# Kernel optimization log

Measured on AMD Instinct MI355X. Metric: run time of the kernel, lower is better.

## Reference

```python
import jax, jax.numpy as jnp
import numpy as np

HIDDEN = 896
N_HEADS = 14
N_KV = 2
HEAD_DIM = HIDDEN // N_HEADS  # 64
N_REP = N_HEADS // N_KV       # 7
ROPE_THETA = 1000000.0


def setup_inputs() -> dict:
    key = jax.random.key(0)
    ks = jax.random.split(key, 8)
    B, S = 2, 2048
    s = 0.02
    return {
        "hidden_states": jax.random.normal(ks[0], (B, S, HIDDEN), dtype=jnp.float32),
        "position_ids": jnp.broadcast_to(jnp.arange(S, dtype=jnp.int64), (B, S)),
        "Wq": jax.random.normal(ks[1], (HIDDEN, HIDDEN), dtype=jnp.float32) * s,
        "bq": jnp.zeros((HIDDEN,), dtype=jnp.float32),
        "Wk": jax.random.normal(ks[2], (N_KV * HEAD_DIM, HIDDEN), dtype=jnp.float32) * s,
        "bk": jnp.zeros((N_KV * HEAD_DIM,), dtype=jnp.float32),
        "Wv": jax.random.normal(ks[3], (N_KV * HEAD_DIM, HIDDEN), dtype=jnp.float32) * s,
        "bv": jnp.zeros((N_KV * HEAD_DIM,), dtype=jnp.float32),
        "Wo": jax.random.normal(ks[4], (HIDDEN, HIDDEN), dtype=jnp.float32) * s,
    }


def _rotate_half(x):
    x1, x2 = x[..., : HEAD_DIM // 2], x[..., HEAD_DIM // 2 :]
    return jnp.concatenate((-x2, x1), axis=-1)


def reference(hidden_states, position_ids, Wq, bq, Wk, bk, Wv, bv, Wo):
    B, S, _ = hidden_states.shape
    q = (hidden_states @ Wq.T + bq).reshape(B, S, N_HEADS, HEAD_DIM)
    k = (hidden_states @ Wk.T + bk).reshape(B, S, N_KV, HEAD_DIM)
    v = (hidden_states @ Wv.T + bv).reshape(B, S, N_KV, HEAD_DIM)

    # RoPE: cos/sin [B, S, 1, HEAD_DIM]
    inv_freq = 1.0 / (ROPE_THETA ** (jnp.arange(0, HEAD_DIM, 2, dtype=jnp.float32) / HEAD_DIM))
    freqs = position_ids.astype(jnp.float32)[..., None] * inv_freq  # [B,S,D/2]
    emb = jnp.concatenate((freqs, freqs), axis=-1)
    cos = jnp.cos(emb)[:, :, None, :]
    sin = jnp.sin(emb)[:, :, None, :]
    q = q * cos + _rotate_half(q) * sin
    k = k * cos + _rotate_half(k) * sin

    # [B, H, S, D]; repeat KV heads (GQA)
    q = q.transpose(0, 2, 1, 3)
    k = jnp.repeat(k.transpose(0, 2, 1, 3), N_REP, axis=1)
    v = jnp.repeat(v.transpose(0, 2, 1, 3), N_REP, axis=1)

    scale = 1.0 / np.sqrt(HEAD_DIM)
    scores = jnp.einsum("bhqd,bhkd->bhqk", q, k) * scale
    causal = jnp.tril(jnp.ones((S, S), dtype=bool))
    scores = jnp.where(causal[None, None, :, :], scores, jnp.finfo(scores.dtype).min)
    probs = jax.nn.softmax(scores, axis=-1)
    attn = jnp.einsum("bhqk,bhkd->bhqd", probs, v)  # [B,H,S,D]
    attn = attn.transpose(0, 2, 1, 3).reshape(B, S, HIDDEN)
    return attn @ Wo.T
```

## Files before the change

### kernel.cpp

```cpp
#include <hip/hip_runtime.h>

#define HID 896
#define NH 14
#define NKV 2
#define NREP 7
#define SEQ 2048
#define BT 2
#define NTOK (BT*SEQ)
#define CSCALE 0.18033688011112042f

typedef __attribute__((ext_vector_type(8))) short bf16x8;
typedef __attribute__((ext_vector_type(8))) unsigned short u16x8;
typedef __attribute__((ext_vector_type(4))) float fx4;
typedef __attribute__((ext_vector_type(4))) short s16x4;
typedef _Float16 f16x4 __attribute__((ext_vector_type(4)));
typedef __fp16 fp16x2 __attribute__((ext_vector_type(2)));

__device__ __forceinline__ unsigned short f2b(float x){
  union { float f; unsigned u; } a; a.f = x;
  unsigned r = a.u + 0x7FFFu + ((a.u >> 16) & 1u);
  return (unsigned short)(r >> 16);
}
__device__ __forceinline__ unsigned short f2h(float x){
  union { _Float16 h; unsigned short u; } a; a.h = (_Float16)x; return a.u;
}

__global__ __launch_bounds__(256) void cvt_kernel(
    const float* __restrict__ s0, const float* __restrict__ s1,
    const float* __restrict__ s2, const float* __restrict__ s3,
    const float* __restrict__ s4,
    unsigned short* __restrict__ d0, unsigned short* __restrict__ d1,
    unsigned short* __restrict__ d2, unsigned short* __restrict__ d3,
    unsigned short* __restrict__ d4,
    int c0, int c1, int c2, int c3, int c4)
{
  const float* s; unsigned short* d; int c;
  switch (blockIdx.y){
    case 0: s=s0; d=d0; c=c0; break;
    case 1: s=s1; d=d1; c=c1; break;
    case 2: s=s2; d=d2; c=c2; break;
    case 3: s=s3; d=d3; c=c3; break;
    default: s=s4; d=d4; c=c4; break;
  }
  for (int i = (blockIdx.x*256 + threadIdx.x)*8; i < c; i += gridDim.x*2048){
    float4 a = *(const float4*)(s + i);
    float4 b = *(const float4*)(s + i + 4);
    u16x8 o;
    o[0]=f2b(a.x); o[1]=f2b(a.y); o[2]=f2b(a.z); o[3]=f2b(a.w);
    o[4]=f2b(b.x); o[5]=f2b(b.y); o[6]=f2b(b.z); o[7]=f2b(b.w);
    *(u16x8*)(d + i) = o;
  }
}

__global__ __launch_bounds__(256) void qkv_gemm_kernel(
    const unsigned short* __restrict__ A, const unsigned short* __restrict__ Bw,
    const float* __restrict__ bq, const float* __restrict__ bk, const float* __restrict__ bv,
    const int* __restrict__ pos,
    unsigned short* __restrict__ qo, unsigned short* __restrict__ ko,
    unsigned short* __restrict__ vt)
{
  __shared__ short As[64*72];
  __shared__ short Bs[128*72];
  const int tid = threadIdx.x;
  const int bm = blockIdx.x, bn = blockIdx.y;
  const int w = tid >> 6, l = tid & 63, l15 = l & 15, q4 = l >> 4;
  const int wm = w >> 1, wn = w & 1;

  fx4 acc[2][4] = {};

  const int srow = tid >> 3, scol = (tid & 7)*8;
  const unsigned short* Ag = A  + (size_t)(bm*64  + srow)*HID + scol;
  const unsigned short* Bg = Bw + (size_t)(bn*128 + srow)*HID + scol;

  u16x8 ar[2], br[4];
#pragma unroll
  for (int p = 0; p < 2; p++) ar[p] = *(const u16x8*)(Ag + (size_t)p*32*HID);
#pragma unroll
  for (int p = 0; p < 4; p++) br[p] = *(const u16x8*)(Bg + (size_t)p*32*HID);

  for (int kt = 0; kt < 14; kt++){
#pragma unroll
    for (int p = 0; p < 2; p++) *(u16x8*)&As[(srow + p*32)*72 + scol] = ar[p];
#pragma unroll
    for (int p = 0; p < 4; p++) *(u16x8*)&Bs[(srow + p*32)*72 + scol] = br[p];
    __syncthreads();
    if (kt < 13){
      const int ko_ = (kt+1)*64;
#pragma unroll
      for (int p = 0; p < 2; p++) ar[p] = *(const u16x8*)(Ag + (size_t)p*32*HID + ko_);
#pragma unroll
      for (int p = 0; p < 4; p++) br[p] = *(const u16x8*)(Bg + (size_t)p*32*HID + ko_);
    }
#pragma unroll
    for (int ks = 0; ks < 2; ks++){
      bf16x8 af[2], bf[4];
#pragma unroll
      for (int mt = 0; mt < 2; mt++)
        af[mt] = *(bf16x8*)&As[(wm*32 + mt*16 + l15)*72 + ks*32 + q4*8];
#pragma unroll
      for (int nt = 0; nt < 4; nt++)
        bf[nt] = *(bf16x8*)&Bs[(wn*64 + nt*16 + l15)*72 + ks*32 + q4*8];
#pragma unroll
      for (int mt = 0; mt < 2; mt++)
#pragma unroll
        for (int nt = 0; nt < 4; nt++)
          acc[mt][nt] = __builtin_amdgcn_mfma_f32_16x16x32_bf16(af[mt], bf[nt], acc[mt][nt], 0,0,0);
    }
    __syncthreads();
  }

  const int hu = bn*2 + wn;
  const float* bias; int kind, hloc;
  if (hu < NH)      { bias = bq + hu*64;      kind = 0; hloc = hu; }
  else if (hu < 16) { bias = bk + (hu-NH)*64; kind = 1; hloc = hu-NH; }
  else              { bias = bv + (hu-16)*64; kind = 2; hloc = hu-16; }
  float bl[4];
#pragma unroll
  for (int nt = 0; nt < 4; nt++) bl[nt] = bias[nt*16 + l15];

  if (kind == 2){
#pragma unroll
    for (int mt = 0; mt < 2; mt++)
#pragma unroll
      for (int j = 0; j < 4; j++){
        int grow = bm*64 + wm*32 + mt*16 + q4*4 + j;
        int b = grow >> 11, s = grow & (SEQ-1);
        int tile = s >> 6, key = s & 63;
        unsigned short* dst = vt + (size_t)(((b*NKV + hloc)*(SEQ/64) + tile)*4096);
#pragma unroll
        for (int nt = 0; nt < 4; nt++)
          dst[(nt*16 + l15)*64 + key] = f2h(acc[mt][nt][j] + bl[nt]);
      }
  } else {
    float invf[2];
#pragma unroll
    for (int nt = 0; nt < 2; nt++)
      invf[nt] = exp2f(-(float)(nt*16 + l15) * 0.62286151779138041f);
#pragma unroll
    for (int mt = 0; mt < 2; mt++)
#pragma unroll
      for (int j = 0; j < 4; j++){
        int grow = bm*64 + wm*32 + mt*16 + q4*4 + j;
        int b = grow >> 11, s = grow & (SEQ-1);
        float p = (float)pos[grow];
        unsigned short* dst = (kind == 0)
            ? qo + ((size_t)(b*NH  + hloc)*SEQ + s)*64
            : ko + ((size_t)(b*NKV + hloc)*SEQ + s)*64;
#pragma unroll
        for (int nt = 0; nt < 2; nt++){
          int d = nt*16 + l15;
          float f = p * invf[nt];
          float sv, cv;
          sincosf(f, &sv, &cv);
          float x1 = acc[mt][nt][j]   + bl[nt];
          float x2 = acc[mt][nt+2][j] + bl[nt+2];
          dst[d]    = f2b(x1*cv - x2*sv);
          dst[d+32] = f2b(x2*cv + x1*sv);
        }
      }
  }
}

__device__ __forceinline__ void smax_pv(
    const fx4* s, bool diag, int wl, int q4,
    float& m_run, float& l_run, fx4* o, const f16x4 vf[4][4])
{
  float tv[16];
#pragma unroll
  for (int tl = 0; tl < 4; tl++)
#pragma unroll
    for (int j = 0; j < 4; j++){
      float x = s[tl][j]*CSCALE;
      if (diag && (tl*16 + q4*4 + j > wl)) x = -1e30f;
      tv[tl*4+j] = x;
    }
  float mx = tv[0];
#pragma unroll
  for (int i = 1; i < 16; i++) mx = fmaxf(mx, tv[i]);
  mx = fmaxf(mx, __shfl_xor(mx, 16));
  mx = fmaxf(mx, __shfl_xor(mx, 32));
  float mn = fmaxf(m_run, mx);
  float al = exp2f(m_run - mn);
  m_run = mn;
  float p[16], rs = 0.f;
#pragma unroll
  for (int i = 0; i < 16; i++){ p[i] = exp2f(tv[i] - mn); rs += p[i]; }
  rs += __shfl_xor(rs, 16);
  rs += __shfl_xor(rs, 32);
  l_run = l_run*al + rs;
#pragma unroll
  for (int nt = 0; nt < 4; nt++)
#pragma unroll
    for (int j = 0; j < 4; j++) o[nt][j] *= al;
  f16x4 pf[4];
#pragma unroll
  for (int tl = 0; tl < 4; tl++){
    union { f16x4 v; fp16x2 h[2]; } u;
    u.h[0] = __builtin_amdgcn_cvt_pkrtz(p[tl*4+0], p[tl*4+1]);
    u.h[1] = __builtin_amdgcn_cvt_pkrtz(p[tl*4+2], p[tl*4+3]);
    pf[tl] = u.v;
  }
#pragma unroll
  for (int nt = 0; nt < 4; nt++)
#pragma unroll
    for (int tl = 0; tl < 4; tl++)
      o[nt] = __builtin_amdgcn_mfma_f32_16x16x16f16(vf[nt][tl], pf[tl], o[nt], 0,0,0);
}

__global__ __launch_bounds__(512) void attn_kernel(
    const unsigned short* __restrict__ q, const unsigned short* __restrict__ k,
    const unsigned short* __restrict__ vt, unsigned short* __restrict__ ao)
{
  __shared__ short SB[4*64*72];
  short* KsB = SB;
  short* VtB = SB + 2*64*72;

  const int tid = threadIdx.x;
  const int w = tid >> 6, l = tid & 63, l15 = l & 15, q4 = l >> 4;
  const int g = w >> 2, wi = w & 3;
  const int tlo = blockIdx.x, thi = 31 - tlo;
  const int h = blockIdx.y, b = blockIdx.z, kvh = h / NREP;
  const int wl = wi*16 + l15;

  const unsigned short* qbase = q + ((size_t)(b*NH + h)*SEQ)*64;
  const unsigned short* qpA = qbase + (size_t)(thi*64 + wl)*64;
  const unsigned short* qpB = qbase + (size_t)(tlo*64 + wl)*64;
  bf16x8 qA0 = *(const bf16x8*)(qpA + q4*8), qA1 = *(const bf16x8*)(qpA + 32 + q4*8);
  bf16x8 qB0 = *(const bf16x8*)(qpB + q4*8), qB1 = *(const bf16x8*)(qpB + 32 + q4*8);

  fx4 oA[4] = {}, oB[4] = {};
  float mA = -1e30f, lA = 0.f, mB = -1e30f, lB = 0.f;

  const unsigned short* kbase = k  + ((size_t)(b*NKV + kvh)*SEQ)*64;
  const unsigned short* vbase = vt + (size_t)((b*NKV + kvh)*(SEQ/64))*4096;

  const int P = (thi + 2) >> 1;

  u16x8 kreg[2], vreg[2];
#pragma unroll
  for (int p = 0; p < 2; p++){
    int idx = p*512 + tid, tile = idx >> 9, off = idx & 511;
    kreg[p] = *(const u16x8*)(kbase + (size_t)tile*4096 + off*8);
    vreg[p] = *(const u16x8*)(vbase + (size_t)tile*4096 + off*8);
  }

  for (int si = 0; si < P; si++){
#pragma unroll
    for (int p = 0; p < 2; p++){
      int idx = p*512 + tid, tile = idx >> 9, off = idx & 511;
      int rr = off >> 3, g8 = off & 7;
      *(u16x8*)&KsB[tile*4608 + rr*72 + g8*8] = kreg[p];
      *(u16x8*)&VtB[tile*4608 + rr*72 + g8*8] = vreg[p];
    }
    __syncthreads();

    if (si + 1 < P){
      const int k0n = 2*(si+1);
#pragma unroll
      for (int p = 0; p < 2; p++){
        int idx = p*512 + tid, tile = idx >> 9, off = idx & 511;
        int tk = k0n + tile; if (tk > thi) tk = thi;
        kreg[p] = *(const u16x8*)(kbase + (size_t)tk*4096 + off*8);
        vreg[p] = *(const u16x8*)(vbase + (size_t)tk*4096 + off*8);
      }
    }

    const int kt = 2*si + g;
    if (kt <= thi){
      const short* Kst = KsB + g*4608;
      const short* Vtt = VtB + g*4608;
      bf16x8 kf0[4], kf1[4];
#pragma unroll
      for (int tl = 0; tl < 4; tl++){
        kf0[tl] = *(const bf16x8*)&Kst[(tl*16 + l15)*72 + q4*8];
        kf1[tl] = *(const bf16x8*)&Kst[(tl*16 + l15)*72 + 32 + q4*8];
      }
      f16x4 vf[4][4];
#pragma unroll
      for (int nt = 0; nt < 4; nt++)
#pragma unroll
        for (int tl = 0; tl < 4; tl++)
          vf[nt][tl] = *(const f16x4*)&Vtt[(nt*16 + l15)*72 + tl*16 + q4*4];

      {
        fx4 s[4] = {};
#pragma unroll
        for (int tl = 0; tl < 4; tl++){
          s[tl] = __builtin_amdgcn_mfma_f32_16x16x32_bf16(kf0[tl], qA0, s[tl], 0,0,0);
          s[tl] = __builtin_amdgcn_mfma_f32_16x16x32_bf16(kf1[tl], qA1, s[tl], 0,0,0);
        }
        smax_pv(s, kt == thi, wl, q4, mA, lA, oA, vf);
      }
      if (kt <= tlo){
        fx4 s[4] = {};
#pragma unroll
        for (int tl = 0; tl < 4; tl++){
          s[tl] = __builtin_amdgcn_mfma_f32_16x16x32_bf16(kf0[tl], qB0, s[tl], 0,0,0);
          s[tl] = __builtin_amdgcn_mfma_f32_16x16x32_bf16(kf1[tl], qB1, s[tl], 0,0,0);
        }
        smax_pv(s, kt == tlo, wl, q4, mB, lB, oB, vf);
      }
    }
    __syncthreads();
  }

  float* F = (float*)SB;
  if (g == 1){
    float* fa = F + (((wi*2 + 0)*64 + l)*18);
#pragma unroll
    for (int nt = 0; nt < 4; nt++)
#pragma unroll
      for (int j = 0; j < 4; j++) fa[nt*4 + j] = oA[nt][j];
    fa[16] = mA; fa[17] = lA;
    float* fb = F + (((wi*2 + 1)*64 + l)*18);
#pragma unroll
    for (int nt = 0; nt < 4; nt++)
#pragma unroll
      for (int j = 0; j < 4; j++) fb[nt*4 + j] = oB[nt][j];
    fb[16] = mB; fb[17] = lB;
  }
  __syncthreads();
  if (g == 0){
    {
      const float* fa = F + (((wi*2 + 0)*64 + l)*18);
      float m1 = fa[16], l1 = fa[17];
      float mM = fmaxf(mA, m1);
      float a0 = exp2f(mA - mM), a1 = exp2f(m1 - mM);
      lA = lA*a0 + l1*a1;
#pragma unroll
      for (int nt = 0; nt < 4; nt++)
#pragma unroll
        for (int j = 0; j < 4; j++) oA[nt][j] = oA[nt][j]*a0 + fa[nt*4+j]*a1;
    }
    {
      const float* fb = F + (((wi*2 + 1)*64 + l)*18);
      float m1 = fb[16], l1 = fb[17];
      float mM = fmaxf(mB, m1);
      float a0 = exp2f(mB - mM), a1 = exp2f(m1 - mM);
      lB = lB*a0 + l1*a1;
#pragma unroll
      for (int nt = 0; nt < 4; nt++)
#pragma unroll
        for (int j = 0; j < 4; j++) oB[nt][j] = oB[nt][j]*a0 + fb[nt*4+j]*a1;
    }
    {
      float inv = 1.0f / lA;
      unsigned short* dst = ao + ((size_t)(b*SEQ + thi*64 + wl))*HID + h*64;
#pragma unroll
      for (int nt = 0; nt < 4; nt++){
        s16x4 ov;
        ov[0] = (short)f2b(oA[nt][0]*inv); ov[1] = (short)f2b(oA[nt][1]*inv);
        ov[2] = (short)f2b(oA[nt][2]*inv); ov[3] = (short)f2b(oA[nt][3]*inv);
        *(s16x4*)(dst + nt*16 + q4*4) = ov;
      }
    }
    {
      float inv = 1.0f / lB;
      unsigned short* dst = ao + ((size_t)(b*SEQ + tlo*64 + wl))*HID + h*64;
#pragma unroll
      for (int nt = 0; nt < 4; nt++){
        s16x4 ov;
        ov[0] = (short)f2b(oB[nt][0]*inv); ov[1] = (short)f2b(oB[nt][1]*inv);
        ov[2] = (short)f2b(oB[nt][2]*inv); ov[3] = (short)f2b(oB[nt][3]*inv);
        *(s16x4*)(dst + nt*16 + q4*4) = ov;
      }
    }
  }
}

__global__ __launch_bounds__(256) void out_gemm_kernel(
    const unsigned short* __restrict__ A, const unsigned short* __restrict__ Bw,
    float* __restrict__ out)
{
  __shared__ short As[64*72];
  __shared__ short Bs[128*72];
  const int tid = threadIdx.x;
  const int bm = blockIdx.x, bn = blockIdx.y;
  const int w = tid >> 6, l = tid & 63, l15 = l & 15, q4 = l >> 4;
  const int wm = w >> 1, wn = w & 1;

  fx4 acc[2][4] = {};

  const int srow = tid >> 3, scol = (tid & 7)*8;
  const unsigned short* Ag = A  + (size_t)(bm*64  + srow)*HID + scol;
  const unsigned short* Bg = Bw + (size_t)(bn*128 + srow)*HID + scol;

  u16x8 ar[2], br[4];
#pragma unroll
  for (int p = 0; p < 2; p++) ar[p] = *(const u16x8*)(Ag + (size_t)p*32*HID);
#pragma unroll
  for (int p = 0; p < 4; p++) br[p] = *(const u16x8*)(Bg + (size_t)p*32*HID);

  for (int kt = 0; kt < 14; kt++){
#pragma unroll
    for (int p = 0; p < 2; p++) *(u16x8*)&As[(srow + p*32)*72 + scol] = ar[p];
#pragma unroll
    for (int p = 0; p < 4; p++) *(u16x8*)&Bs[(srow + p*32)*72 + scol] = br[p];
    __syncthreads();
    if (kt < 13){
      const int ko_ = (kt+1)*64;
#pragma unroll
      for (int p = 0; p < 2; p++) ar[p] = *(const u16x8*)(Ag + (size_t)p*32*HID + ko_);
#pragma unroll
      for (int p = 0; p < 4; p++) br[p] = *(const u16x8*)(Bg + (size_t)p*32*HID + ko_);
    }
#pragma unroll
    for (int ks = 0; ks < 2; ks++){
      bf16x8 af[2], bf[4];
#pragma unroll
      for (int mt = 0; mt < 2; mt++)
        af[mt] = *(bf16x8*)&As[(wm*32 + mt*16 + l15)*72 + ks*32 + q4*8];
#pragma unroll
      for (int nt = 0; nt < 4; nt++)
        bf[nt] = *(bf16x8*)&Bs[(wn*64 + nt*16 + l15)*72 + ks*32 + q4*8];
#pragma unroll
      for (int mt = 0; mt < 2; mt++)
#pragma unroll
        for (int nt = 0; nt < 4; nt++)
          acc[mt][nt] = __builtin_amdgcn_mfma_f32_16x16x32_bf16(af[mt], bf[nt], acc[mt][nt], 0,0,0);
    }
    __syncthreads();
  }

#pragma unroll
  for (int mt = 0; mt < 2; mt++)
#pragma unroll
    for (int j = 0; j < 4; j++){
      int grow = bm*64 + wm*32 + mt*16 + q4*4 + j;
      float* dst = out + (size_t)grow*HID + bn*128 + wn*64;
#pragma unroll
      for (int nt = 0; nt < 4; nt++)
        dst[nt*16 + l15] = acc[mt][nt][j];
    }
}

extern "C" void kernel_launch(void* const* d_in, const int* in_sizes, int n_in,
                              void* d_out, int out_size, void* d_ws, size_t ws_size,
                              hipStream_t stream)
{
  const float* hidden = (const float*)d_in[0];
  const int*   pos    = (const int*)d_in[1];
  const float* Wq = (const float*)d_in[2]; const float* bq = (const float*)d_in[3];
  const float* Wk = (const float*)d_in[4]; const float* bk = (const float*)d_in[5];
  const float* Wv = (const float*)d_in[6]; const float* bv = (const float*)d_in[7];
  const float* Wo = (const float*)d_in[8];

  unsigned short* qws   = (unsigned short*)d_ws;
  unsigned short* kws   = qws   + (size_t)BT*NH*SEQ*64;
  unsigned short* vtws  = kws   + (size_t)BT*NKV*SEQ*64;
  unsigned short* wqkv  = vtws  + (size_t)BT*NKV*SEQ*64;
  unsigned short* wo16  = wqkv  + (size_t)1152*HID;
  unsigned short* h16   = wo16  + (size_t)HID*HID;

  const int nh   = NTOK*HID;
  const int nwq  = HID*HID;
  const int nwkv = 2*64*HID;

  cvt_kernel<<<dim3(448, 5), 256, 0, stream>>>(
      hidden, Wq, Wk, Wv, Wo,
      h16, wqkv, wqkv + nwq, wqkv + nwq + nwkv, wo16,
      nh, nwq, nwkv, nwkv, nwq);

  qkv_gemm_kernel<<<dim3(NTOK/64, 9), 256, 0, stream>>>(
      h16, wqkv, bq, bk, bv, pos, qws, kws, vtws);

  attn_kernel<<<dim3(16, NH, BT), 512, 0, stream>>>(qws, kws, vtws, h16 );

  out_gemm_kernel<<<dim3(NTOK/64, 7), 256, 0, stream>>>(h16 , wo16, (float*)d_out);
}
```

Before: 171.7 us.

## Fuse hidden conversion into QKV GEMM, precompute RoPE table, unpair attention tiles

The fp32 hidden states are now converted to bf16 inside the QKV GEMM's shared-memory staging, which removes the separate conversion pass. The conversion kernel instead builds a cos/sin table that the GEMM epilogue reads rather than calling sincosf per element. The softmax scale is folded into Q at projection time. The attention kernel no longer pairs a low and a high query tile per block; it launches one block per tile, which doubles the grid and may lose the load balancing the pairing provided. The RoPE table is indexed by position id, so it assumes positions are below SEQ.

Result: slower. 195.9 us (+14.0%).

```diff
diff --git a/kernel.cpp b/kernel.cpp
--- a/kernel.cpp
+++ b/kernel.cpp
@@ -28,19 +28,26 @@
 __global__ __launch_bounds__(256) void cvt_kernel(
     const float* __restrict__ s0, const float* __restrict__ s1,
     const float* __restrict__ s2, const float* __restrict__ s3,
-    const float* __restrict__ s4,
     unsigned short* __restrict__ d0, unsigned short* __restrict__ d1,
     unsigned short* __restrict__ d2, unsigned short* __restrict__ d3,
-    unsigned short* __restrict__ d4,
-    int c0, int c1, int c2, int c3, int c4)
-{
+    int c0, int c1, int c2, int c3,
+    float2* __restrict__ tab)
+{
+  if (blockIdx.y == 4){
+    for (int i = blockIdx.x*256 + threadIdx.x; i < SEQ*32; i += gridDim.x*256){
+      int s = i >> 5, d = i & 31;
+      float f = (float)s * exp2f(-(float)d * 0.62286151779138041f);
+      float sv, cv; sincosf(f, &sv, &cv);
+      tab[i] = make_float2(cv, sv);
+    }
+    return;
+  }
   const float* s; unsigned short* d; int c;
   switch (blockIdx.y){
     case 0: s=s0; d=d0; c=c0; break;
     case 1: s=s1; d=d1; c=c1; break;
     case 2: s=s2; d=d2; c=c2; break;
-    case 3: s=s3; d=d3; c=c3; break;
-    default: s=s4; d=d4; c=c4; break;
+    default: s=s3; d=d3; c=c3; break;
   }
   for (int i = (blockIdx.x*256 + threadIdx.x)*8; i < c; i += gridDim.x*2048){
     float4 a = *(const float4*)(s + i);
@@ -53,9 +60,9 @@
 }
 
 __global__ __launch_bounds__(256) void qkv_gemm_kernel(
-    const unsigned short* __restrict__ A, const unsigned short* __restrict__ Bw,
+    const float* __restrict__ hidden, const unsigned short* __restrict__ Bw,
     const float* __restrict__ bq, const float* __restrict__ bk, const float* __restrict__ bv,
-    const int* __restrict__ pos,
+    const int* __restrict__ pos, const float2* __restrict__ tab,
     unsigned short* __restrict__ qo, unsigned short* __restrict__ ko,
     unsigned short* __restrict__ vt)
 {
@@ -69,25 +76,36 @@
   fx4 acc[2][4] = {};
 
   const int srow = tid >> 3, scol = (tid & 7)*8;
-  const unsigned short* Ag = A  + (size_t)(bm*64  + srow)*HID + scol;
+  const float* Agf = hidden + (size_t)(bm*64 + srow)*HID + scol;
   const unsigned short* Bg = Bw + (size_t)(bn*128 + srow)*HID + scol;
 
-  u16x8 ar[2], br[4];
-#pragma unroll
-  for (int p = 0; p < 2; p++) ar[p] = *(const u16x8*)(Ag + (size_t)p*32*HID);
+  float4 a0[2], a1[2]; u16x8 br[4];
+#pragma unroll
+  for (int p = 0; p < 2; p++){
+    a0[p] = *(const float4*)(Agf + (size_t)p*32*HID);
+    a1[p] = *(const float4*)(Agf + (size_t)p*32*HID + 4);
+  }
 #pragma unroll
   for (int p = 0; p < 4; p++) br[p] = *(const u16x8*)(Bg + (size_t)p*32*HID);
 
   for (int kt = 0; kt < 14; kt++){
 #pragma unroll
-    for (int p = 0; p < 2; p++) *(u16x8*)&As[(srow + p*32)*72 + scol] = ar[p];
+    for (int p = 0; p < 2; p++){
+      u16x8 av;
+      av[0]=f2b(a0[p].x); av[1]=f2b(a0[p].y); av[2]=f2b(a0[p].z); av[3]=f2b(a0[p].w);
+      av[4]=f2b(a1[p].x); av[5]=f2b(a1[p].y); av[6]=f2b(a1[p].z); av[7]=f2b(a1[p].w);
+      *(u16x8*)&As[(srow + p*32)*72 + scol] = av;
+    }
 #pragma unroll
     for (int p = 0; p < 4; p++) *(u16x8*)&Bs[(srow + p*32)*72 + scol] = br[p];
     __syncthreads();
     if (kt < 13){
       const int ko_ = (kt+1)*64;
 #pragma unroll
-      for (int p = 0; p < 2; p++) ar[p] = *(const u16x8*)(Ag + (size_t)p*32*HID + ko_);
+      for (int p = 0; p < 2; p++){
+        a0[p] = *(const float4*)(Agf + (size_t)p*32*HID + ko_);
+        a1[p] = *(const float4*)(Agf + (size_t)p*32*HID + ko_ + 4);
+      }
 #pragma unroll
       for (int p = 0; p < 4; p++) br[p] = *(const u16x8*)(Bg + (size_t)p*32*HID + ko_);
     }
@@ -132,31 +150,25 @@
           dst[(nt*16 + l15)*64 + key] = f2h(acc[mt][nt][j] + bl[nt]);
       }
   } else {
-    float invf[2];
-#pragma unroll
-    for (int nt = 0; nt < 2; nt++)
-      invf[nt] = exp2f(-(float)(nt*16 + l15) * 0.62286151779138041f);
+    const float qs = (kind == 0) ? CSCALE : 1.0f;
 #pragma unroll
     for (int mt = 0; mt < 2; mt++)
 #pragma unroll
       for (int j = 0; j < 4; j++){
         int grow = bm*64 + wm*32 + mt*16 + q4*4 + j;
         int b = grow >> 11, s = grow & (SEQ-1);
-        float p = (float)pos[grow];
+        int p = pos[grow];
+        const float2* rp = tab + p*32 + l15;
+        float2 cs0 = rp[0], cs1 = rp[16];
         unsigned short* dst = (kind == 0)
             ? qo + ((size_t)(b*NH  + hloc)*SEQ + s)*64
             : ko + ((size_t)(b*NKV + hloc)*SEQ + s)*64;
-#pragma unroll
-        for (int nt = 0; nt < 2; nt++){
-          int d = nt*16 + l15;
-          float f = p * invf[nt];
-          float sv, cv;
-          sincosf(f, &sv, &cv);
-          float x1 = acc[mt][nt][j]   + bl[nt];
-          float x2 = acc[mt][nt+2][j] + bl[nt+2];
-          dst[d]    = f2b(x1*cv - x2*sv);
-          dst[d+32] = f2b(x2*cv + x1*sv);
-        }
+        float x1 = acc[mt][0][j] + bl[0], x2 = acc[mt][2][j] + bl[2];
+        float y1 = acc[mt][1][j] + bl[1], y2 = acc[mt][3][j] + bl[3];
+        dst[l15]      = f2b((x1*cs0.x - x2*cs0.y)*qs);
+        dst[16 + l15] = f2b((y1*cs1.x - y2*cs1.y)*qs);
+        dst[32 + l15] = f2b((x2*cs0.x + x1*cs0.y)*qs);
+        dst[48 + l15] = f2b((y2*cs1.x + y1*cs1.y)*qs);
       }
   }
 }
@@ -170,7 +182,7 @@
   for (int tl = 0; tl < 4; tl++)
 #pragma unroll
     for (int j = 0; j < 4; j++){
-      float x = s[tl][j]*CSCALE;
+      float x = s[tl][j];
       if (diag && (tl*16 + q4*4 + j > wl)) x = -1e30f;
       tv[tl*4+j] = x;
     }
@@ -218,30 +230,28 @@
   const int tid = threadIdx.x;
   const int w = tid >> 6, l = tid & 63, l15 = l & 15, q4 = l >> 4;
   const int g = w >> 2, wi = w & 3;
-  const int tlo = blockIdx.x, thi = 31 - tlo;
+  const int t = 31 - (int)blockIdx.x;
   const int h = blockIdx.y, b = blockIdx.z, kvh = h / NREP;
   const int wl = wi*16 + l15;
 
-  const unsigned short* qbase = q + ((size_t)(b*NH + h)*SEQ)*64;
-  const unsigned short* qpA = qbase + (size_t)(thi*64 + wl)*64;
-  const unsigned short* qpB = qbase + (size_t)(tlo*64 + wl)*64;
-  bf16x8 qA0 = *(const bf16x8*)(qpA + q4*8), qA1 = *(const bf16x8*)(qpA + 32 + q4*8);
-  bf16x8 qB0 = *(const bf16x8*)(qpB + q4*8), qB1 = *(const bf16x8*)(qpB + 32 + q4*8);
-
-  fx4 oA[4] = {}, oB[4] = {};
-  float mA = -1e30f, lA = 0.f, mB = -1e30f, lB = 0.f;
+  const unsigned short* qp = q + ((size_t)(b*NH + h)*SEQ + t*64 + wl)*64;
+  bf16x8 qf0 = *(const bf16x8*)(qp + q4*8), qf1 = *(const bf16x8*)(qp + 32 + q4*8);
+
+  fx4 o[4] = {};
+  float m_run = -1e30f, l_run = 0.f;
 
   const unsigned short* kbase = k  + ((size_t)(b*NKV + kvh)*SEQ)*64;
   const unsigned short* vbase = vt + (size_t)((b*NKV + kvh)*(SEQ/64))*4096;
 
-  const int P = (thi + 2) >> 1;
+  const int P = (t + 2) >> 1;
 
   u16x8 kreg[2], vreg[2];
 #pragma unroll
   for (int p = 0; p < 2; p++){
     int idx = p*512 + tid, tile = idx >> 9, off = idx & 511;
-    kreg[p] = *(const u16x8*)(kbase + (size_t)tile*4096 + off*8);
-    vreg[p] = *(const u16x8*)(vbase + (size_t)tile*4096 + off*8);
+    int tk = tile > t ? t : tile;
+    kreg[p] = *(const u16x8*)(kbase + (size_t)tk*4096 + off*8);
+    vreg[p] = *(const u16x8*)(vbase + (size_t)tk*4096 + off*8);
   }
 
   for (int si = 0; si < P; si++){
@@ -259,14 +269,14 @@
 #pragma unroll
       for (int p = 0; p < 2; p++){
         int idx = p*512 + tid, tile = idx >> 9, off = idx & 511;
-        int tk = k0n + tile; if (tk > thi) tk = thi;
+        int tk = k0n + tile; if (tk > t) tk = t;
         kreg[p] = *(const u16x8*)(kbase + (size_t)tk*4096 + off*8);
         vreg[p] = *(const u16x8*)(vbase + (size_t)tk*4096 + off*8);
       }
     }
 
     const int kt = 2*si + g;
-    if (kt <= thi){
+    if (kt <= t){
       const short* Kst = KsB + g*4608;
       const short* Vtt = VtB + g*4608;
       bf16x8 kf0[4], kf1[4];
@@ -282,88 +292,46 @@
         for (int tl = 0; tl < 4; tl++)
           vf[nt][tl] = *(const f16x4*)&Vtt[(nt*16 + l15)*72 + tl*16 + q4*4];
 
-      {
-        fx4 s[4] = {};
-#pragma unroll
-        for (int tl = 0; tl < 4; tl++){
-          s[tl] = __builtin_amdgcn_mfma_f32_16x16x32_bf16(kf0[tl], qA0, s[tl], 0,0,0);
-          s[tl] = __builtin_amdgcn_mfma_f32_16x16x32_bf16(kf1[tl], qA1, s[tl], 0,0,0);
-        }
-        smax_pv(s, kt == thi, wl, q4, mA, lA, oA, vf);
-      }
-      if (kt <= tlo){
-        fx4 s[4] = {};
-#pragma unroll
-        for (int tl = 0; tl < 4; tl++){
-          s[tl] = __builtin_amdgcn_mfma_f32_16x16x32_bf16(kf0[tl], qB0, s[tl], 0,0,0);
-          s[tl] = __builtin_amdgcn_mfma_f32_16x16x32_bf16(kf1[tl], qB1, s[tl], 0,0,0);
-        }
-        smax_pv(s, kt == tlo, wl, q4, mB, lB, oB, vf);
-      }
+      fx4 s[4] = {};
+#pragma unroll
+      for (int tl = 0; tl < 4; tl++){
+        s[tl] = __builtin_amdgcn_mfma_f32_16x16x32_bf16(kf0[tl], qf0, s[tl], 0,0,0);
+        s[tl] = __builtin_amdgcn_mfma_f32_16x16x32_bf16(kf1[tl], qf1, s[tl], 0,0,0);
+      }
+      smax_pv(s, kt == t, wl, q4, m_run, l_run, o, vf);
     }
     __syncthreads();
   }
 
   float* F = (float*)SB;
   if (g == 1){
-    float* fa = F + (((wi*2 + 0)*64 + l)*18);
+    float* f = F + ((wi*64 + l)*18);
 #pragma unroll
     for (int nt = 0; nt < 4; nt++)
 #pragma unroll
-      for (int j = 0; j < 4; j++) fa[nt*4 + j] = oA[nt][j];
-    fa[16] = mA; fa[17] = lA;
-    float* fb = F + (((wi*2 + 1)*64 + l)*18);
-#pragma unroll
-    for (int nt = 0; nt < 4; nt++)
-#pragma unroll
-      for (int j = 0; j < 4; j++) fb[nt*4 + j] = oB[nt][j];
-    fb[16] = mB; fb[17] = lB;
+      for (int j = 0; j < 4; j++) f[nt*4 + j] = o[nt][j];
+    f[16] = m_run; f[17] = l_run;
   }
   __syncthreads();
   if (g == 0){
-    {
-      const float* fa = F + (((wi*2 + 0)*64 + l)*18);
-      float m1 = fa[16], l1 = fa[17];
-      float mM = fmaxf(mA, m1);
-      float a0 = exp2f(mA - mM), a1 = exp2f(m1 - mM);
-      lA = lA*a0 + l1*a1;
-#pragma unroll
-      for (int nt = 0; nt < 4; nt++)
-#pragma unroll
-        for (int j = 0; j < 4; j++) oA[nt][j] = oA[nt][j]*a0 + fa[nt*4+j]*a1;
-    }
-    {
-      const float* fb = F + (((wi*2 + 1)*64 + l)*18);
-      float m1 = fb[16], l1 = fb[17];
-      float mM = fmaxf(mB, m1);
-      float a0 = exp2f(mB - mM), a1 = exp2f(m1 - mM);
-      lB = lB*a0 + l1*a1;
-#pragma unroll
-      for (int nt = 0; nt < 4; nt++)
-#pragma unroll
-        for (int j = 0; j < 4; j++) oB[nt][j] = oB[nt][j]*a0 + fb[nt*4+j]*a1;
-    }
-    {
-      float inv = 1.0f / lA;
-      unsigned short* dst = ao + ((size_t)(b*SEQ + thi*64 + wl))*HID + h*64;
-#pragma unroll
-      for (int nt = 0; nt < 4; nt++){
-        s16x4 ov;
-        ov[0] = (short)f2b(oA[nt][0]*inv); ov[1] = (short)f2b(oA[nt][1]*inv);
-        ov[2] = (short)f2b(oA[nt][2]*inv); ov[3] = (short)f2b(oA[nt][3]*inv);
-        *(s16x4*)(dst + nt*16 + q4*4) = ov;
-      }
-    }
-    {
-      float inv = 1.0f / lB;
-      unsigned short* dst = ao + ((size_t)(b*SEQ + tlo*64 + wl))*HID + h*64;
-#pragma unroll
-      for (int nt = 0; nt < 4; nt++){
-        s16x4 ov;
-        ov[0] = (short)f2b(oB[nt][0]*inv); ov[1] = (short)f2b(oB[nt][1]*inv);
-        ov[2] = (short)f2b(oB[nt][2]*inv); ov[3] = (short)f2b(oB[nt][3]*inv);
-        *(s16x4*)(dst + nt*16 + q4*4) = ov;
-      }
+    const float* f = F + ((wi*64 + l)*18);
+    float m1 = f[16], l1 = f[17];
+    float mM = fmaxf(m_run, m1);
+    float a0 = exp2f(m_run - mM), a1 = exp2f(m1 - mM);
+    l_run = l_run*a0 + l1*a1;
+#pragma unroll
+    for (int nt = 0; nt < 4; nt++)
+#pragma unroll
+      for (int j = 0; j < 4; j++) o[nt][j] = o[nt][j]*a0 + f[nt*4+j]*a1;
+
+    float inv = 1.0f / l_run;
+    unsigned short* dst = ao + ((size_t)(b*SEQ + t*64 + wl))*HID + h*64;
+#pragma unroll
+    for (int nt = 0; nt < 4; nt++){
+      s16x4 ov;
+      ov[0] = (short)f2b(o[nt][0]*inv); ov[1] = (short)f2b(o[nt][1]*inv);
+      ov[2] = (short)f2b(o[nt][2]*inv); ov[3] = (short)f2b(o[nt][3]*inv);
+      *(s16x4*)(dst + nt*16 + q4*4) = ov;
     }
   }
 }
@@ -451,20 +419,20 @@
   unsigned short* wqkv  = vtws  + (size_t)BT*NKV*SEQ*64;
   unsigned short* wo16  = wqkv  + (size_t)1152*HID;
   unsigned short* h16   = wo16  + (size_t)HID*HID;
-
-  const int nh   = NTOK*HID;
+  float2*         tab   = (float2*)(h16 + (size_t)NTOK*HID);
+
   const int nwq  = HID*HID;
   const int nwkv = 2*64*HID;
 
-  cvt_kernel<<<dim3(448, 5), 256, 0, stream>>>(
-      hidden, Wq, Wk, Wv, Wo,
-      h16, wqkv, wqkv + nwq, wqkv + nwq + nwkv, wo16,
-      nh, nwq, nwkv, nwkv, nwq);
+  cvt_kernel<<<dim3(392, 5), 256, 0, stream>>>(
+      Wq, Wk, Wv, Wo,
+      wqkv, wqkv + nwq, wqkv + nwq + nwkv, wo16,
+      nwq, nwkv, nwkv, nwq, tab);
 
   qkv_gemm_kernel<<<dim3(NTOK/64, 9), 256, 0, stream>>>(
-      h16, wqkv, bq, bk, bv, pos, qws, kws, vtws);
-
-  attn_kernel<<<dim3(16, NH, BT), 512, 0, stream>>>(qws, kws, vtws, h16 );
-
-  out_gemm_kernel<<<dim3(NTOK/64, 7), 256, 0, stream>>>(h16 , wo16, (float*)d_out);
-}
+      hidden, wqkv, bq, bk, bv, pos, tab, qws, kws, vtws);
+
+  attn_kernel<<<dim3(32, NH, BT), 512, 0, stream>>>(qws, kws, vtws, h16);
+
+  out_gemm_kernel<<<dim3(NTOK/64, 7), 256, 0, stream>>>(h16, wo16, (float*)d_out);
+}
```
